# Performance work log

Hardware: AMD Instinct MI355X
Metric: run time of the kernel (lower is better)

The kernel has to match this reference:

```python
import jax, jax.numpy as jnp
import numpy as np
from jax import lax

WINDOW_SIZE = 7
SIGMA = 1.5
C1 = 0.01 ** 2
C2 = 0.03 ** 2


def gaussian_window3d(window_size: int, channel: int) -> jnp.ndarray:
    g = jnp.arange(window_size, dtype=jnp.float32) - window_size // 2
    g = jnp.exp(-g ** 2 / (2.0 * SIGMA ** 2))
    g = g / g.sum()  # [k]
    w3 = g[:, None, None] * g[None, :, None] * g[None, None, :]  # [k,k,k]
    # OIDHW layout for depthwise conv: [channel, 1, k, k, k]
    return jnp.broadcast_to(w3[None, None], (channel, 1, window_size, window_size, window_size))


def depthwise_conv3d(x, window):
    # x: [N,C,D,H,W]; window: [C,1,k,k,k]; SAME padding via pad = k//2
    k = window.shape[-1]
    p = k // 2
    return lax.conv_general_dilated(
        x, window,
        window_strides=(1, 1, 1),
        padding=[(p, p)] * 3,
        dimension_numbers=('NCDHW', 'OIDHW', 'NCDHW'),
        feature_group_count=x.shape[1],
    )


def setup_inputs() -> dict:
    key = jax.random.key(0)
    k1, k2 = jax.random.split(key)
    shape = (2, 1, 160, 256, 256)
    img1 = jax.random.uniform(k1, shape, dtype=jnp.float32)
    img2 = jax.random.uniform(k2, shape, dtype=jnp.float32)
    window = gaussian_window3d(WINDOW_SIZE, shape[1])
    return {"img1": img1, "img2": img2, "window": window}


def reference(img1, img2, window):
    mu1 = depthwise_conv3d(img1, window)
    mu2 = depthwise_conv3d(img2, window)
    mu1_sq = mu1 * mu1
    mu2_sq = mu2 * mu2
    mu1_mu2 = mu1 * mu2
    sigma1_sq = depthwise_conv3d(img1 * img1, window) - mu1_sq
    sigma2_sq = depthwise_conv3d(img2 * img2, window) - mu2_sq
    sigma12 = depthwise_conv3d(img1 * img2, window) - mu1_mu2
    ssim_map = ((2.0 * mu1_mu2 + C1) * (2.0 * sigma12 + C2)) / (
        (mu1_sq + mu2_sq + C1) * (sigma1_sq + sigma2_sq + C2)
    )
    return ssim_map.mean()  # size_average=True
```

## Files before the change

### kernel.cpp

```cpp
#include <hip/hip_runtime.h>
#include <math.h>

#define HW 65536
#define DD 160
#define NB 2
#define DCH 40
#define NSL (DCH + 6)
#define NCH 4
#define TW 32
#define TH 16
#define PH 23

#define SSIM_C1 1e-4f
#define SSIM_C2 9e-4f

typedef float f32x2 __attribute__((ext_vector_type(2)));

struct Gw { float g[7]; };

static __device__ __forceinline__ f32x2 s2(float v) { f32x2 r; r.x = v; r.y = v; return r; }

__global__ __launch_bounds__(256, 2) void k_fused(
    const float* __restrict__ img1, const float* __restrict__ img2,
    Gw gw, float* __restrict__ partials)
{
    __shared__ f32x2 pA[2][TW][PH];
    __shared__ f32x2 pB[2][TW][PH];
    __shared__ float pC[2][TW][PH];
    __shared__ float red[256];

    const int tid = threadIdx.x;
    const int nb = blockIdx.z >> 2;
    const int o0 = (blockIdx.z & 3) * DCH;
    const int h0 = blockIdx.y * TH;
    const int w0 = blockIdx.x * TW;
    const float* i1 = img1 + (size_t)nb * DD * HW;
    const float* i2 = img2 + (size_t)nb * DD * HW;

    const bool wth = (tid < 176);
    const int hh = tid >> 3;
    const int wb = (tid & 7) * 4;
    const int gh = h0 - 3 + hh;
    const int gwb = w0 - 3 + wb;
    const bool ghv = wth && ((unsigned)gh < 256u);
    const int ghc = gh < 0 ? 0 : (gh > 255 ? 255 : gh);
    int coff[10];
    float mx[10];
#pragma unroll
    for (int i = 0; i < 10; ++i) {
        int gwi = gwb + i;
        int gc = gwi < 0 ? 0 : (gwi > 255 ? 255 : gwi);
        coff[i] = ghc * 256 + gc;
        mx[i] = (ghv && gwi == gc) ? 1.f : 0.f;
    }

    const int wcol = tid & 31;
    const int hb = (tid >> 5) * 2;

    f32x2 ringA[2][7] = {};
    f32x2 ringB[2][7] = {};
    float ringC[2][7] = {};
    float lsum = 0.f;
    f32x2 cA[10], cB[10];

    auto LOADTO = [&](f32x2 (&buf)[10], int s) {
        const float* p1 = i1 + (size_t)s * HW;
        const float* p2 = i2 + (size_t)s * HW;
#pragma unroll
        for (int i = 0; i < 10; ++i) buf[i].x = p1[coff[i]];
#pragma unroll
        for (int i = 0; i < 10; ++i) buf[i].y = p2[coff[i]];
    };

    {
        const int s0 = o0 - 3;
        if (s0 >= 0 && wth) LOADTO(cA, s0);
        const int s1 = o0 - 2;
        if (s1 >= 0 && wth) LOADTO(cB, s1);
    }

#define PHASE(Q, CUR)                                                         \
    {                                                                         \
        const int r = 14 * t2 + (Q);                                          \
        if (r <= NSL) {                                                       \
            const int scur = o0 - 3 + r;                                      \
            const bool wv = (r < NSL) && (scur >= 0) && (scur < DD);          \
                        \
            if (wv && wth) {                                                  \
                f32x2 aA[4] = {};                                             \
                f32x2 aB[4] = {};                                             \
                float aC[4] = {};                                             \
                _Pragma("unroll")                                             \
                for (int i = 0; i < 10; ++i) {                                \
                    const f32x2 xi2 = CUR[i] * s2(mx[i]);                     \
                    const f32x2 xx2 = xi2 * xi2;                              \
                    const float xy = xi2.x * xi2.y;                           \
                    _Pragma("unroll")                                         \
                    for (int o = 0; o < 4; ++o) {                             \
                        const int k = i - o;                                  \
                        if (k >= 0 && k < 7) {                                \
                            const float gk = gw.g[k];                         \
                            aA[o] += s2(gk) * xi2;                            \
                            aB[o] += s2(gk) * xx2;                            \
                            aC[o] += gk * xy;                                 \
                        }                                                     \
                    }                                                         \
                }                                                             \
                _Pragma("unroll")                                             \
                for (int o = 0; o < 4; ++o) {                                 \
                    pA[(Q) & 1][wb + o][hh] = aA[o];                          \
                    pB[(Q) & 1][wb + o][hh] = aB[o];                          \
                    pC[(Q) & 1][wb + o][hh] = aC[o];                          \
                }                                                             \
            }                                                                 \
               \
            {                                                                 \
                const int sn2 = scur + 2;                                     \
                if ((r + 2 < NSL) && (sn2 >= 0) && (sn2 < DD) && wth)         \
                    LOADTO(CUR, sn2);                                         \
            }                                                                 \
             \
            if (r >= 1) {                                                     \
                const int rp = r - 1;                                         \
                const int sp = o0 - 3 + rp;                                   \
                if (sp >= 0 && sp < DD) {                                     \
                    f32x2 vA[8], vB[8];                                       \
                    float vC[8];                                              \
                    _Pragma("unroll")                                         \
                    for (int i = 0; i < 8; ++i) {                             \
                        vA[i] = pA[((Q) + 1) & 1][wcol][hb + i];              \
                        vB[i] = pB[((Q) + 1) & 1][wcol][hb + i];              \
                        vC[i] = pC[((Q) + 1) & 1][wcol][hb + i];              \
                    }                                                         \
                    _Pragma("unroll")                                         \
                    for (int o = 0; o < 2; ++o) {                             \
                        f32x2 aA = s2(0.f), aB = s2(0.f);                     \
                        float aC = 0.f;                                       \
                        _Pragma("unroll")                                     \
                        for (int k = 0; k < 7; ++k) {                         \
                            const float gk = gw.g[k];                         \
                            aA += s2(gk) * vA[o + k];                         \
                            aB += s2(gk) * vB[o + k];                         \
                            aC += gk * vC[o + k];                             \
                        }                                                     \
                        ringA[o][((Q) + 6) % 7] = aA;                         \
                        ringB[o][((Q) + 6) % 7] = aB;                         \
                        ringC[o][((Q) + 6) % 7] = aC;                         \
                    }                                                         \
                } else {                                                      \
                    _Pragma("unroll")                                         \
                    for (int o = 0; o < 2; ++o) {                             \
                        ringA[o][((Q) + 6) % 7] = s2(0.f);                    \
                        ringB[o][((Q) + 6) % 7] = s2(0.f);                    \
                        ringC[o][((Q) + 6) % 7] = 0.f;                        \
                    }                                                         \
                }                                                             \
                if (r >= 7) {                                                 \
                    f32x2 CAq[2], CBq[2];                                     \
                    float CCq[2];                                             \
                    _Pragma("unroll")                                         \
                    for (int o = 0; o < 2; ++o) {                             \
                        f32x2 cAa = s2(0.f), cBa = s2(0.f);                   \
                        float cCa = 0.f;                                      \
                        _Pragma("unroll")                                     \
                        for (int k = 0; k < 7; ++k) {                         \
                            const float gk = gw.g[k];                         \
                            const int pp = (((Q) + 6) % 7 + 1 + k) % 7;       \
                            cAa += s2(gk) * ringA[o][pp];                     \
                            cBa += s2(gk) * ringB[o][pp];                     \
                            cCa += gk * ringC[o][pp];                         \
                        }                                                     \
                        CAq[o] = cAa; CBq[o] = cBa; CCq[o] = cCa;             \
                    }                                                         \
                    f32x2 mu1, mu2, E11, E22, E12;                            \
                    mu1.x = CAq[0].x; mu1.y = CAq[1].x;                       \
                    mu2.x = CAq[0].y; mu2.y = CAq[1].y;                       \
                    E11.x = CBq[0].x; E11.y = CBq[1].x;                       \
                    E22.x = CBq[0].y; E22.y = CBq[1].y;                       \
                    E12.x = CCq[0];   E12.y = CCq[1];                         \
                    const f32x2 mu1s = mu1 * mu1;                             \
                    const f32x2 mu2s = mu2 * mu2;                             \
                    const f32x2 m12 = mu1 * mu2;                              \
                    const f32x2 sg1 = E11 - mu1s;                             \
                    const f32x2 sg2 = E22 - mu2s;                             \
                    const f32x2 s12 = E12 - m12;                              \
                    const f32x2 num = (s2(2.f) * m12 + s2(SSIM_C1)) *         \
                                      (s2(2.f) * s12 + s2(SSIM_C2));          \
                    const f32x2 den = (mu1s + mu2s + s2(SSIM_C1)) *           \
                                      (sg1 + sg2 + s2(SSIM_C2));              \
                    lsum += num.x * __builtin_amdgcn_rcpf(den.x)              \
                          + num.y * __builtin_amdgcn_rcpf(den.y);             \
                }                                                             \
            }                                                                 \
            __syncthreads();                                                  \
        }                                                                     \
    }

    for (int t2 = 0; t2 < 4; ++t2) {
        PHASE(0, cA)  PHASE(1, cB)  PHASE(2, cA)  PHASE(3, cB)
        PHASE(4, cA)  PHASE(5, cB)  PHASE(6, cA)  PHASE(7, cB)
        PHASE(8, cA)  PHASE(9, cB)  PHASE(10, cA) PHASE(11, cB)
        PHASE(12, cA) PHASE(13, cB)
    }
#undef PHASE

    red[tid] = lsum;
    __syncthreads();
    for (int off = 128; off > 0; off >>= 1) {
        if (tid < off) red[tid] += red[tid + off];
        __syncthreads();
    }
    if (tid == 0)
        partials[(blockIdx.z * gridDim.y + blockIdx.y) * gridDim.x + blockIdx.x] = red[0];
}

__global__ __launch_bounds__(256) void k_final(
    const float* __restrict__ partials, int n, float scale, float* __restrict__ out)
{
    __shared__ float red[256];
    float s = 0.f;
    for (int i = threadIdx.x; i < n; i += 256) s += partials[i];
    red[threadIdx.x] = s;
    __syncthreads();
    for (int off = 128; off > 0; off >>= 1) {
        if (threadIdx.x < off) red[threadIdx.x] += red[threadIdx.x + off];
        __syncthreads();
    }
    if (threadIdx.x == 0) out[0] = red[0] * scale;
}

extern "C" void kernel_launch(void* const* d_in, const int* in_sizes, int n_in,
                              void* d_out, int out_size, void* d_ws, size_t ws_size,
                              hipStream_t stream)
{
    const float* img1 = (const float*)d_in[0];
    const float* img2 = (const float*)d_in[1];
    float* out = (float*)d_out;
    float* partials = (float*)d_ws;

    Gw gw;
    {
        double gs[7], sum = 0.0;
        for (int i = 0; i < 7; ++i) { double x = i - 3; gs[i] = exp(-x * x / 4.5); sum += gs[i]; }
        for (int i = 0; i < 7; ++i) gw.g[i] = (float)(gs[i] / sum);
    }

    dim3 grid(256 / TW, 256 / TH, NB * NCH);
    k_fused<<<grid, dim3(256), 0, stream>>>(img1, img2, gw, partials);
    k_final<<<dim3(1), dim3(256), 0, stream>>>(
        partials, (256 / TW) * (256 / TH) * NB * NCH, (float)(1.0 / 20971520.0), out);
}
```

Baseline: 153.1 us.

## Convolve sum/difference images to cut filtered channels from five to four

Replaces the five convolved quantities (x, y, x², y², xy) with four: u=x+y, v=x−y and their squares. The SSIM terms are then rebuilt algebraically from the filtered u, v, u² and v². This removes one channel from every separable convolution pass, from the shared-memory staging buffers and from the register ring buffers, which cuts FMAs, LDS traffic and register pressure. The cost is a few extra adds per voxel and some change in floating-point rounding from the sum/difference form.

```diff
diff --git a/kernel.cpp b/kernel.cpp
--- a/kernel.cpp
+++ b/kernel.cpp
@@ -24,9 +24,8 @@
     const float* __restrict__ img1, const float* __restrict__ img2,
     Gw gw, float* __restrict__ partials)
 {
-    __shared__ f32x2 pA[2][TW][PH];
-    __shared__ f32x2 pB[2][TW][PH];
-    __shared__ float pC[2][TW][PH];
+    __shared__ f32x2 pUV[2][TW][PH];
+    __shared__ f32x2 pSQ[2][TW][PH];
     __shared__ float red[256];
 
     const int tid = threadIdx.x;
@@ -57,9 +56,8 @@
     const int wcol = tid & 31;
     const int hb = (tid >> 5) * 2;
 
-    f32x2 ringA[2][7] = {};
-    f32x2 ringB[2][7] = {};
-    float ringC[2][7] = {};
+    f32x2 ringUV[2][7] = {};
+    f32x2 ringSQ[2][7] = {};
     float lsum = 0.f;
     f32x2 cA[10], cB[10];
 
@@ -87,30 +85,29 @@
             const bool wv = (r < NSL) && (scur >= 0) && (scur < DD);          \
                         \
             if (wv && wth) {                                                  \
-                f32x2 aA[4] = {};                                             \
-                f32x2 aB[4] = {};                                             \
-                float aC[4] = {};                                             \
+                f32x2 aUV[4] = {};                                            \
+                f32x2 aSQ[4] = {};                                            \
                 _Pragma("unroll")                                             \
                 for (int i = 0; i < 10; ++i) {                                \
-                    const f32x2 xi2 = CUR[i] * s2(mx[i]);                     \
-                    const f32x2 xx2 = xi2 * xi2;                              \
-                    const float xy = xi2.x * xi2.y;                           \
+                    f32x2 uv;                                                 \
+                    uv.x = CUR[i].x + CUR[i].y;                               \
+                    uv.y = CUR[i].x - CUR[i].y;                               \
+                    uv = uv * s2(mx[i]);                                      \
+                    const f32x2 sq = uv * uv;                                 \
                     _Pragma("unroll")                                         \
                     for (int o = 0; o < 4; ++o) {                             \
                         const int k = i - o;                                  \
                         if (k >= 0 && k < 7) {                                \
                             const float gk = gw.g[k];                         \
-                            aA[o] += s2(gk) * xi2;                            \
-                            aB[o] += s2(gk) * xx2;                            \
-                            aC[o] += gk * xy;                                 \
+                            aUV[o] += s2(gk) * uv;                            \
+                            aSQ[o] += s2(gk) * sq;                            \
                         }                                                     \
                     }                                                         \
                 }                                                             \
                 _Pragma("unroll")                                             \
                 for (int o = 0; o < 4; ++o) {                                 \
-                    pA[(Q) & 1][wb + o][hh] = aA[o];                          \
-                    pB[(Q) & 1][wb + o][hh] = aB[o];                          \
-                    pC[(Q) & 1][wb + o][hh] = aC[o];                          \
+                    pUV[(Q) & 1][wb + o][hh] = aUV[o];                        \
+                    pSQ[(Q) & 1][wb + o][hh] = aSQ[o];                        \
                 }                                                             \
             }                                                                 \
                \
@@ -124,72 +121,55 @@
                 const int rp = r - 1;                                         \
                 const int sp = o0 - 3 + rp;                                   \
                 if (sp >= 0 && sp < DD) {                                     \
-                    f32x2 vA[8], vB[8];                                       \
-                    float vC[8];                                              \
+                    f32x2 vU[8], vS[8];                                       \
                     _Pragma("unroll")                                         \
                     for (int i = 0; i < 8; ++i) {                             \
-                        vA[i] = pA[((Q) + 1) & 1][wcol][hb + i];              \
-                        vB[i] = pB[((Q) + 1) & 1][wcol][hb + i];              \
-                        vC[i] = pC[((Q) + 1) & 1][wcol][hb + i];              \
+                        vU[i] = pUV[((Q) + 1) & 1][wcol][hb + i];             \
+                        vS[i] = pSQ[((Q) + 1) & 1][wcol][hb + i];             \
                     }                                                         \
                     _Pragma("unroll")                                         \
                     for (int o = 0; o < 2; ++o) {                             \
-                        f32x2 aA = s2(0.f), aB = s2(0.f);                     \
-                        float aC = 0.f;                                       \
+                        f32x2 aU = s2(0.f), aS = s2(0.f);                     \
                         _Pragma("unroll")                                     \
                         for (int k = 0; k < 7; ++k) {                         \
                             const float gk = gw.g[k];                         \
-                            aA += s2(gk) * vA[o + k];                         \
-                            aB += s2(gk) * vB[o + k];                         \
-                            aC += gk * vC[o + k];                             \
+                            aU += s2(gk) * vU[o + k];                         \
+                            aS += s2(gk) * vS[o + k];                         \
                         }                                                     \
-                        ringA[o][((Q) + 6) % 7] = aA;                         \
-                        ringB[o][((Q) + 6) % 7] = aB;                         \
-                        ringC[o][((Q) + 6) % 7] = aC;                         \
+                        ringUV[o][((Q) + 6) % 7] = aU;                        \
+                        ringSQ[o][((Q) + 6) % 7] = aS;                        \
                     }                                                         \
                 } else {                                                      \
                     _Pragma("unroll")                                         \
                     for (int o = 0; o < 2; ++o) {                             \
-                        ringA[o][((Q) + 6) % 7] = s2(0.f);                    \
-                        ringB[o][((Q) + 6) % 7] = s2(0.f);                    \
-                        ringC[o][((Q) + 6) % 7] = 0.f;                        \
+                        ringUV[o][((Q) + 6) % 7] = s2(0.f);                   \
+                        ringSQ[o][((Q) + 6) % 7] = s2(0.f);                   \
                     }                                                         \
                 }                                                             \
                 if (r >= 7) {                                                 \
-                    f32x2 CAq[2], CBq[2];                                     \
-                    float CCq[2];                                             \
                     _Pragma("unroll")                                         \
                     for (int o = 0; o < 2; ++o) {                             \
-                        f32x2 cAa = s2(0.f), cBa = s2(0.f);                   \
-                        float cCa = 0.f;                                      \
+                        f32x2 cU = s2(0.f), cS = s2(0.f);                     \
                         _Pragma("unroll")                                     \
                         for (int k = 0; k < 7; ++k) {                         \
                             const float gk = gw.g[k];                         \
                             const int pp = (((Q) + 6) % 7 + 1 + k) % 7;       \
-                            cAa += s2(gk) * ringA[o][pp];                     \
-                            cBa += s2(gk) * ringB[o][pp];                     \
-                            cCa += gk * ringC[o][pp];                         \
+                            cU += s2(gk) * ringUV[o][pp];                     \
+                            cS += s2(gk) * ringSQ[o][pp];                     \
                         }                                                     \
-                        CAq[o] = cAa; CBq[o] = cBa; CCq[o] = cCa;             \
-                    }                                                         \
-                    f32x2 mu1, mu2, E11, E22, E12;                            \
-                    mu1.x = CAq[0].x; mu1.y = CAq[1].x;                       \
-                    mu2.x = CAq[0].y; mu2.y = CAq[1].y;                       \
-                    E11.x = CBq[0].x; E11.y = CBq[1].x;                       \
-                    E22.x = CBq[0].y; E22.y = CBq[1].y;                       \
-                    E12.x = CCq[0];   E12.y = CCq[1];                         \
-                    const f32x2 mu1s = mu1 * mu1;                             \
-                    const f32x2 mu2s = mu2 * mu2;                             \
-                    const f32x2 m12 = mu1 * mu2;                              \
-                    const f32x2 sg1 = E11 - mu1s;                             \
-                    const f32x2 sg2 = E22 - mu2s;                             \
-                    const f32x2 s12 = E12 - m12;                              \
-                    const f32x2 num = (s2(2.f) * m12 + s2(SSIM_C1)) *         \
-                                      (s2(2.f) * s12 + s2(SSIM_C2));          \
-                    const f32x2 den = (mu1s + mu2s + s2(SSIM_C1)) *           \
-                                      (sg1 + sg2 + s2(SSIM_C2));              \
-                    lsum += num.x * __builtin_amdgcn_rcpf(den.x)              \
-                          + num.y * __builtin_amdgcn_rcpf(den.y);             \
+                          \
+                        const f32x2 ab2 = cU * cU;                            \
+                        const float sAB = ab2.x + ab2.y;                      \
+                        const float dAB = ab2.x - ab2.y;                      \
+                        const float sPQ = cS.x + cS.y;                        \
+                        const float dPQ = cS.x - cS.y;                        \
+                        const float num1 = 0.5f * dAB + SSIM_C1;              \
+                        const float num2 = 0.5f * (dPQ - dAB) + SSIM_C2;      \
+                        const float den1 = 0.5f * sAB + SSIM_C1;              \
+                        const float den2 = 0.5f * (sPQ - sAB) + SSIM_C2;      \
+                        lsum += (num1 * num2) *                               \
+                                __builtin_amdgcn_rcpf(den1 * den2);           \
+                    }                                                         \
                 }                                                             \
             }                                                                 \
             __syncthreads();                                                  \
```

Result: no change. 151.6 us (median of 3 runs) (-1.0%).
